# Performance work log

Hardware: AMD Instinct MI355X
Metric: run time of the kernel (lower is better)

Reference implementation:

```python
import jax, jax.numpy as jnp
import numpy as np

B, C, H, W = 8, 128, 64, 64  # dim = in_channels = 128, N = H*W = 4096
TEMP = float(C) ** 0.5


def _proj(x, w, b):
    # 1x1 conv: [B,C,H,W] x [D,C] -> [B,D,H,W]
    return jnp.einsum('bchw,dc->bdhw', x, w) + b[None, :, None, None]


def setup_inputs() -> dict:
    key = jax.random.key(0)
    ks = jax.random.split(key, 6)
    std = 0.01
    x = jax.random.normal(ks[0], (B, C, H, W), dtype=jnp.float32)
    wq = jax.random.normal(ks[1], (C, C), dtype=jnp.float32) * std
    wk = jax.random.normal(ks[2], (C, C), dtype=jnp.float32) * std
    wv = jax.random.normal(ks[3], (C, C), dtype=jnp.float32) * std
    wo = jax.random.normal(ks[4], (C, C), dtype=jnp.float32) * std
    zeros = jnp.zeros((C,), dtype=jnp.float32)
    return {"x": x, "wq": wq, "bq": zeros, "wk": wk, "bk": zeros,
            "wv": wv, "bv": zeros, "wo": wo, "bo": zeros}


def reference(x, wq, bq, wk, bk, wv, bv, wo, bo):
    n, c, h, w = x.shape
    N = h * w
    q = _proj(x, wq, bq).reshape(n, c, N)          # [B, D, N]
    k = _proj(x, wk, bk).reshape(n, c, N)          # [B, D, N]
    v = _proj(x, wv, bv).reshape(n, c, N)          # [B, D, N]
    # attn[b, i, j] = sum_d q[b,d,i] * k[b,d,j] / temp
    attn = jnp.einsum('bdi,bdj->bij', q, k) / TEMP  # [B, N, N]
    attn = jax.nn.softmax(attn, axis=-1)
    # y[b, d, i] = sum_j attn[b,i,j] * v[b,d,j]
    y = jnp.einsum('bij,bdj->bdi', attn, v).reshape(n, c, h, w)
    y = _proj(y, wo, bo)                            # conv_out
    return x + y                                    # identity residual
```

## Files before the change

kernel.cpp:

```cpp
#include <hip/hip_runtime.h>


typedef float  f32x4  __attribute__((ext_vector_type(4)));
typedef float  f32x16 __attribute__((ext_vector_type(16)));
typedef short  s16x8  __attribute__((ext_vector_type(8)));
typedef short  s16x4  __attribute__((ext_vector_type(4)));
typedef unsigned uint4v __attribute__((ext_vector_type(4)));

#define MFMA16(A, Bb, Cc) __builtin_amdgcn_mfma_f32_16x16x32_bf16(A, Bb, Cc, 0, 0, 0)
#define MFMA32(A, Bb, Cc) __builtin_amdgcn_mfma_f32_32x32x16_bf16(A, Bb, Cc, 0, 0, 0)

#define BATCH 8
#define DIM   128
#define NN    4096
#define NSPLIT 4
#define JCHUNK (NN / NSPLIT)
#define Q_SCALE 0.12751649736784776f

__device__ __forceinline__ unsigned short f2bf(float f) {
  union { float f; unsigned u; } v; v.f = f;
  unsigned r = v.u + 0x7FFFu + ((v.u >> 16) & 1u);
  return (unsigned short)(r >> 16);
}
__device__ __forceinline__ float bf2f(unsigned short h) {
  union { unsigned u; float f; } v; v.u = ((unsigned)h) << 16;
  return v.f;
}
__device__ __forceinline__ s16x8 cvt8(const float* src) {
  float4 a = *(const float4*)src;
  float4 b = *(const float4*)(src + 4);
  s16x8 f;
  f[0] = (short)f2bf(a.x); f[1] = (short)f2bf(a.y);
  f[2] = (short)f2bf(a.z); f[3] = (short)f2bf(a.w);
  f[4] = (short)f2bf(b.x); f[5] = (short)f2bf(b.y);
  f[6] = (short)f2bf(b.z); f[7] = (short)f2bf(b.w);
  return f;
}

__global__ __launch_bounds__(256) void qkv_kernel(
    const float* __restrict__ x,
    const float* __restrict__ wq, const float* __restrict__ wk,
    const float* __restrict__ wv,
    const float* __restrict__ bq, const float* __restrict__ bk,
    const float* __restrict__ bv,
    unsigned short* __restrict__ qt,
    unsigned short* __restrict__ kt,
    unsigned short* __restrict__ vv) {
  __shared__ float xs[DIM * 68];
  __shared__ unsigned short wls[DIM * 136];
  const int b = blockIdx.y;
  const int i0 = blockIdx.x * 64;
  const int tid = threadIdx.x;

  for (int idx = tid; idx < 2048; idx += 256) {
    int c = idx >> 4, i4 = idx & 15;
    float4 val = *(const float4*)(x + ((size_t)(b * DIM + c)) * NN + i0 + i4 * 4);
    xs[c * 68 + i4 * 4 + 0] = val.x;
    xs[c * 68 + i4 * 4 + 1] = val.y;
    xs[c * 68 + i4 * 4 + 2] = val.z;
    xs[c * 68 + i4 * 4 + 3] = val.w;
  }
  __syncthreads();

  const int w = tid >> 6, lane = tid & 63, quad = lane >> 4, l15 = lane & 15;
  const int iloc = w * 16 + l15;

  s16x8 bfrag[4];
#pragma unroll
  for (int ch = 0; ch < 4; ch++) {
    s16x8 f;
#pragma unroll
    for (int jj = 0; jj < 8; jj++) {
      int c = ch * 32 + quad * 8 + jj;
      f[jj] = (short)f2bf(xs[c * 68 + iloc]);
    }
    bfrag[ch] = f;
  }

  const int i = i0 + iloc;
  const int wr = tid >> 4, wc = tid & 15;

  for (int z = 0; z < 3; z++) {
    __syncthreads();
    const float* wsrc = (z == 0) ? wq : (z == 1) ? wk : wv;
#pragma unroll
    for (int it = 0; it < 8; it++) {
      const int row = it * 16 + wr;
      *(s16x8*)(&wls[row * 136 + wc * 8]) = cvt8(wsrc + row * DIM + wc * 8);
    }
    __syncthreads();

    const float* bias = (z == 0) ? bq : (z == 1) ? bk : bv;
    const float sc = (z == 0) ? Q_SCALE : 1.0f;

    for (int t = 0; t < 8; t++) {
      const int dl = t * 16;
      f32x4 acc = {0.f, 0.f, 0.f, 0.f};
#pragma unroll
      for (int ch = 0; ch < 4; ch++) {
        s16x8 af = *(const s16x8*)(&wls[(dl + l15) * 136 + ch * 32 + quad * 8]);
        acc = MFMA16(af, bfrag[ch], acc);
      }
      if (z < 2) {
        unsigned short* dstb = (z == 0) ? qt : kt;
        s16x4 o;
#pragma unroll
        for (int r = 0; r < 4; r++) {
          int d = dl + quad * 4 + r;
          o[r] = (short)f2bf((acc[r] + bias[d]) * sc);
        }
        *(s16x4*)(dstb + ((size_t)b * NN + i) * DIM + dl + quad * 4) = o;
      } else {
#pragma unroll
        for (int r = 0; r < 4; r++) {
          int d = dl + quad * 4 + r;
          vv[((size_t)b * DIM + d) * NN + i] = f2bf(acc[r] + bias[d]);
        }
      }
    }
  }
}

__global__ __launch_bounds__(256, 2) void attn_kernel(
    const unsigned short* __restrict__ qt,
    const unsigned short* __restrict__ kt,
    const unsigned short* __restrict__ vv,
    unsigned short* __restrict__ o_part,
    float* __restrict__ l_part) {
  __shared__ unsigned short sh[16384];
  const int b = blockIdx.y;
  const int i0 = blockIdx.x * 128;
  const int split = blockIdx.z;
  const int jbase = split * JCHUNK;
  const int tid = threadIdx.x;
  const int w = tid >> 6, lane = tid & 63;
  const int l31 = lane & 31, h = lane >> 5;

  const unsigned short* kb = kt + (size_t)b * NN * DIM;
  const unsigned short* vb = vv + (size_t)b * DIM * NN;

  s16x8 qfrag[8];
  {
    const unsigned short* qrow =
        qt + ((size_t)b * NN + i0 + w * 32 + l31) * DIM + h * 8;
#pragma unroll
    for (int kc = 0; kc < 8; kc++)
      qfrag[kc] = *(const s16x8*)(qrow + kc * 16);
  }

  f32x16 acc[4];
#pragma unroll
  for (int mt = 0; mt < 4; mt++)
#pragma unroll
    for (int e = 0; e < 16; e++) acc[mt][e] = 0.f;
  float l_acc = 0.f;

  const int kr = tid >> 4, kc_ = tid & 15;
  const int vr = tid >> 3, vc = tid & 7;
  const int vch0 = (vc & 1) ? (vc - 1) : vc;
  const int vch1 = (vc & 1) ? vc : (vc + 1);
  const int vpos = (vc & 1) * 4;

  s16x8 kpre[4], vpre[4];
#pragma unroll
  for (int it = 0; it < 4; it++) {
    kpre[it] = *(const s16x8*)(kb + (size_t)(jbase + it * 16 + kr) * DIM + kc_ * 8);
    vpre[it] = *(const s16x8*)(vb + (size_t)(it * 32 + vr) * NN + jbase + vc * 8);
  }

  for (int j0 = jbase; j0 < jbase + JCHUNK; j0 += 64) {
    __syncthreads();
#pragma unroll
    for (int it = 0; it < 4; it++) {
      const int r = it * 16 + kr;
      *(s16x8*)(sh + (((r << 4) + (kc_ ^ (r & 15))) << 3)) = kpre[it];
      const int r2 = it * 32 + vr;
      union { s16x8 v8; s16x4 v4[2]; } sp; sp.v8 = vpre[it];
      *(s16x4*)(sh + 8192 + (((r2 << 3) + (vch0 ^ (r2 & 7))) << 3) + vpos) = sp.v4[0];
      *(s16x4*)(sh + 8192 + (((r2 << 3) + (vch1 ^ (r2 & 7))) << 3) + vpos) = sp.v4[1];
    }
    __syncthreads();

    if (j0 + 64 < jbase + JCHUNK) {
      const int jn = j0 + 64;
#pragma unroll
      for (int it = 0; it < 4; it++) {
        kpre[it] = *(const s16x8*)(kb + (size_t)(jn + it * 16 + kr) * DIM + kc_ * 8);
        vpre[it] = *(const s16x8*)(vb + (size_t)(it * 32 + vr) * NN + jn + vc * 8);
      }
    }

#pragma unroll
    for (int jt = 0; jt < 2; jt++) {
      f32x16 S;
#pragma unroll
      for (int e = 0; e < 16; e++) S[e] = 0.f;
      const int j = jt * 32 + l31;
#pragma unroll
      for (int kc = 0; kc < 8; kc++) {
        s16x8 kf = *(const s16x8*)(sh + (((j << 4) + ((2 * kc + h) ^ (j & 15))) << 3));
        S = MFMA32(kf, qfrag[kc], S);
      }
      unsigned pk[8];
#pragma unroll
      for (int p = 0; p < 8; p++) {
        float e0 = exp2f(S[2 * p]), e1 = exp2f(S[2 * p + 1]);
        l_acc += e0 + e1;
        union { float f; unsigned u; } u0, u1; u0.f = e0; u1.f = e1;
        pk[p] = __builtin_amdgcn_perm(u1.u, u0.u, 0x07060302u);
      }
#pragma unroll
      for (int bl = 0; bl < 2; bl++) {
        union { uint4v u; s16x8 v; } pu;
        pu.u[0] = pk[4 * bl + 0]; pu.u[1] = pk[4 * bl + 1];
        pu.u[2] = pk[4 * bl + 2]; pu.u[3] = pk[4 * bl + 3];
        const s16x8 pf = pu.v;
        const int c0 = (jt * 2 + bl) * 2 + h;
#pragma unroll
        for (int mt = 0; mt < 4; mt++) {
          const int d = mt * 32 + l31;
          s16x8 vf = *(const s16x8*)(sh + 8192 + (((d << 3) + (c0 ^ (d & 7))) << 3));
          acc[mt] = MFMA32(vf, pf, acc[mt]);
        }
      }
    }
  }

  const float l_tot = l_acc + __shfl_xor(l_acc, 32, 64);

  __syncthreads();
  unsigned short* ep = sh + w * 4096;
#pragma unroll
  for (int mt = 0; mt < 4; mt++)
#pragma unroll
    for (int reg = 0; reg < 16; reg++) {
      int d = mt * 32 + (reg & 3) + 8 * (reg >> 2) + 4 * h;
      int dc = d >> 3;
      ep[(l31 << 7) + ((dc ^ (l31 & 15)) << 3) + (d & 7)] = f2bf(acc[mt][reg]);
    }
  __syncthreads();
#pragma unroll
  for (int it = 0; it < 8; it++) {
    int qr = it * 4 + (lane >> 4), cr = lane & 15;
    s16x8 v = *(const s16x8*)(ep + (qr << 7) + ((cr ^ (qr & 15)) << 3));
    *(s16x8*)(o_part + (((size_t)split * BATCH + b) * NN + i0 + w * 32 + qr) * DIM +
              cr * 8) = v;
  }
  if (lane < 32)
    l_part[((size_t)split * BATCH + b) * NN + i0 + w * 32 + lane] = l_tot;
}

__global__ __launch_bounds__(256) void outp_kernel(
    const float* __restrict__ x,
    const float* __restrict__ wo,
    const float* __restrict__ bo,
    const unsigned short* __restrict__ o_part,
    const float* __restrict__ l_part,
    float* __restrict__ out) {
  __shared__ unsigned short ytile[64 * 136];
  __shared__ unsigned short wls[DIM * 136];
  __shared__ float invl[64];
  const int b = blockIdx.y;
  const int i0 = blockIdx.x * 64;
  const int tid = threadIdx.x;
  const int wr = tid >> 4, wc = tid & 15;

#pragma unroll
  for (int it = 0; it < 8; it++) {
    const int row = it * 16 + wr;
    *(s16x8*)(&wls[row * 136 + wc * 8]) = cvt8(wo + row * DIM + wc * 8);
  }

  if (tid < 64) {
    float l = 0.f;
#pragma unroll
    for (int s = 0; s < NSPLIT; s++)
      l += l_part[((size_t)s * BATCH + b) * NN + i0 + tid];
    invl[tid] = 1.0f / l;
  }
  __syncthreads();

#pragma unroll
  for (int k = 0; k < 4; k++) {
    int slot = k * 256 + tid;
    int i = slot >> 4, g = slot & 15;
    float o[8] = {0.f, 0.f, 0.f, 0.f, 0.f, 0.f, 0.f, 0.f};
#pragma unroll
    for (int s = 0; s < NSPLIT; s++) {
      s16x8 ov = *(const s16x8*)(o_part +
                                 (((size_t)s * BATCH + b) * NN + i0 + i) * DIM + g * 8);
#pragma unroll
      for (int jj = 0; jj < 8; jj++) o[jj] += bf2f((unsigned short)ov[jj]);
    }
    const float inv = invl[i];
    s16x8 f;
#pragma unroll
    for (int jj = 0; jj < 8; jj++) f[jj] = (short)f2bf(o[jj] * inv);
    *(s16x8*)(&ytile[i * 136 + g * 8]) = f;
  }
  __syncthreads();

  const int w = tid >> 6, lane = tid & 63, quad = lane >> 4, l15 = lane & 15;
  const int i = i0 + w * 16 + l15;

  s16x8 bfrag[4];
#pragma unroll
  for (int ch = 0; ch < 4; ch++)
    bfrag[ch] = *(const s16x8*)(&ytile[(w * 16 + l15) * 136 + ch * 32 + quad * 8]);

  for (int t = 0; t < 8; t++) {
    f32x4 acc = {0.f, 0.f, 0.f, 0.f};
#pragma unroll
    for (int ch = 0; ch < 4; ch++) {
      s16x8 af = *(const s16x8*)(&wls[(t * 16 + l15) * 136 + ch * 32 + quad * 8]);
      acc = MFMA16(af, bfrag[ch], acc);
    }
#pragma unroll
    for (int r = 0; r < 4; r++) {
      int d = t * 16 + quad * 4 + r;
      size_t idx = ((size_t)b * DIM + d) * NN + i;
      out[idx] = x[idx] + acc[r] + bo[d];
    }
  }
}

extern "C" void kernel_launch(void* const* d_in, const int* in_sizes, int n_in,
                              void* d_out, int out_size, void* d_ws, size_t ws_size,
                              hipStream_t stream) {
  const float* x  = (const float*)d_in[0];
  const float* wq = (const float*)d_in[1];
  const float* bq = (const float*)d_in[2];
  const float* wk = (const float*)d_in[3];
  const float* bk = (const float*)d_in[4];
  const float* wv = (const float*)d_in[5];
  const float* bv = (const float*)d_in[6];
  const float* wo = (const float*)d_in[7];
  const float* bo = (const float*)d_in[8];
  float* out = (float*)d_out;

  unsigned short* ws  = (unsigned short*)d_ws;
  unsigned short* qt  = ws;
  unsigned short* kt  = qt + (size_t)BATCH * NN * DIM;
  unsigned short* vv  = kt + (size_t)BATCH * NN * DIM;
  unsigned short* o_part = vv + (size_t)BATCH * NN * DIM;
  float* l_part = (float*)(o_part + (size_t)NSPLIT * BATCH * NN * DIM);

  hipLaunchKernelGGL(qkv_kernel, dim3(64, 8), dim3(256), 0, stream,
                     x, wq, wk, wv, bq, bk, bv, qt, kt, vv);
  hipLaunchKernelGGL(attn_kernel, dim3(32, 8, NSPLIT), dim3(256), 0, stream,
                     qt, kt, vv, o_part, l_part);
  hipLaunchKernelGGL(outp_kernel, dim3(64, 8), dim3(256), 0, stream,
                     x, wo, bo, o_part, l_part, out);
}
```

Baseline: 182.6 us.

## Store K in MFMA-fragment tiled layout and read it directly from global

The projection kernel now writes K into a per-64-row tiled layout matching the MFMA operand fragment order. The attention kernel loads K fragments straight from global/L2 instead of staging them through shared memory, which removes the K LDS writes and reads. The split count over the key dimension also drops from 4 to 2, halving the number of blocks and partial outputs. The trade-off is that K loads are now issued directly in the inner loop with no prefetch, so their latency may be exposed.

```diff
diff --git a/kernel.cpp b/kernel.cpp
--- a/kernel.cpp
+++ b/kernel.cpp
@@ -13,7 +13,7 @@
 #define BATCH 8
 #define DIM   128
 #define NN    4096
-#define NSPLIT 4
+#define NSPLIT 2
 #define JCHUNK (NN / NSPLIT)
 #define Q_SCALE 0.12751649736784776f
 
@@ -79,6 +79,7 @@
 
   const int i = i0 + iloc;
   const int wr = tid >> 4, wc = tid & 15;
+  unsigned short* ktb = kt + ((size_t)b * 64 + blockIdx.x) * 16384;
 
   for (int z = 0; z < 3; z++) {
     __syncthreads();
@@ -101,15 +102,24 @@
         s16x8 af = *(const s16x8*)(&wls[(dl + l15) * 136 + ch * 32 + quad * 8]);
         acc = MFMA16(af, bfrag[ch], acc);
       }
-      if (z < 2) {
-        unsigned short* dstb = (z == 0) ? qt : kt;
+      if (z == 0) {
         s16x4 o;
 #pragma unroll
         for (int r = 0; r < 4; r++) {
           int d = dl + quad * 4 + r;
           o[r] = (short)f2bf((acc[r] + bias[d]) * sc);
         }
-        *(s16x4*)(dstb + ((size_t)b * NN + i) * DIM + dl + quad * 4) = o;
+        *(s16x4*)(qt + ((size_t)b * NN + i) * DIM + dl + quad * 4) = o;
+      } else if (z == 1) {
+        s16x4 o;
+#pragma unroll
+        for (int r = 0; r < 4; r++) {
+          int d = dl + quad * 4 + r;
+          o[r] = (short)f2bf(acc[r] + bias[d]);
+        }
+        const int c = t * 2 + (quad >> 1);
+        const int e = (quad & 1) * 4;
+        *(s16x4*)(ktb + ((size_t)c * 64 + iloc) * 8 + e) = o;
       } else {
 #pragma unroll
         for (int r = 0; r < 4; r++) {
@@ -136,8 +146,9 @@
   const int w = tid >> 6, lane = tid & 63;
   const int l31 = lane & 31, h = lane >> 5;
 
-  const unsigned short* kb = kt + (size_t)b * NN * DIM;
   const unsigned short* vb = vv + (size_t)b * DIM * NN;
+  const unsigned short* ktile = kt + ((size_t)b * 64 + (jbase >> 6)) * 16384;
+  const int koff = (h * 64 + l31) * 8;
 
   s16x8 qfrag[8];
   {
@@ -155,39 +166,32 @@
     for (int e = 0; e < 16; e++) acc[mt][e] = 0.f;
   float l_acc = 0.f;
 
-  const int kr = tid >> 4, kc_ = tid & 15;
   const int vr = tid >> 3, vc = tid & 7;
   const int vch0 = (vc & 1) ? (vc - 1) : vc;
   const int vch1 = (vc & 1) ? vc : (vc + 1);
   const int vpos = (vc & 1) * 4;
 
-  s16x8 kpre[4], vpre[4];
-#pragma unroll
-  for (int it = 0; it < 4; it++) {
-    kpre[it] = *(const s16x8*)(kb + (size_t)(jbase + it * 16 + kr) * DIM + kc_ * 8);
+  s16x8 vpre[4];
+#pragma unroll
+  for (int it = 0; it < 4; it++)
     vpre[it] = *(const s16x8*)(vb + (size_t)(it * 32 + vr) * NN + jbase + vc * 8);
-  }
 
   for (int j0 = jbase; j0 < jbase + JCHUNK; j0 += 64) {
     __syncthreads();
 #pragma unroll
     for (int it = 0; it < 4; it++) {
-      const int r = it * 16 + kr;
-      *(s16x8*)(sh + (((r << 4) + (kc_ ^ (r & 15))) << 3)) = kpre[it];
       const int r2 = it * 32 + vr;
       union { s16x8 v8; s16x4 v4[2]; } sp; sp.v8 = vpre[it];
-      *(s16x4*)(sh + 8192 + (((r2 << 3) + (vch0 ^ (r2 & 7))) << 3) + vpos) = sp.v4[0];
-      *(s16x4*)(sh + 8192 + (((r2 << 3) + (vch1 ^ (r2 & 7))) << 3) + vpos) = sp.v4[1];
+      *(s16x4*)(sh + (((r2 << 3) + (vch0 ^ (r2 & 7))) << 3) + vpos) = sp.v4[0];
+      *(s16x4*)(sh + (((r2 << 3) + (vch1 ^ (r2 & 7))) << 3) + vpos) = sp.v4[1];
     }
     __syncthreads();
 
     if (j0 + 64 < jbase + JCHUNK) {
       const int jn = j0 + 64;
 #pragma unroll
-      for (int it = 0; it < 4; it++) {
-        kpre[it] = *(const s16x8*)(kb + (size_t)(jn + it * 16 + kr) * DIM + kc_ * 8);
+      for (int it = 0; it < 4; it++)
         vpre[it] = *(const s16x8*)(vb + (size_t)(it * 32 + vr) * NN + jn + vc * 8);
-      }
     }
 
 #pragma unroll
@@ -195,10 +199,9 @@
       f32x16 S;
 #pragma unroll
       for (int e = 0; e < 16; e++) S[e] = 0.f;
-      const int j = jt * 32 + l31;
 #pragma unroll
       for (int kc = 0; kc < 8; kc++) {
-        s16x8 kf = *(const s16x8*)(sh + (((j << 4) + ((2 * kc + h) ^ (j & 15))) << 3));
+        s16x8 kf = *(const s16x8*)(ktile + kc * 1024 + jt * 256 + koff);
         S = MFMA32(kf, qfrag[kc], S);
       }
       unsigned pk[8];
@@ -219,11 +222,12 @@
 #pragma unroll
         for (int mt = 0; mt < 4; mt++) {
           const int d = mt * 32 + l31;
-          s16x8 vf = *(const s16x8*)(sh + 8192 + (((d << 3) + (c0 ^ (d & 7))) << 3));
+          s16x8 vf = *(const s16x8*)(sh + (((d << 3) + (c0 ^ (d & 7))) << 3));
           acc[mt] = MFMA32(vf, pf, acc[mt]);
         }
       }
     }
+    ktile += 16384;
   }
 
   const float l_tot = l_acc + __shfl_xor(l_acc, 32, 64);
```

Result: slower. 209.8 us (+14.9%).
